# Kernel optimization log

Hardware: AMD Instinct MI355X
Metric: run time of the kernel (lower is better)

Reference implementation:

```python
import jax, jax.numpy as jnp
import numpy as np

B, T, F = 4, 8192, 1024
K = 4  # kernel_size

def setup_inputs() -> dict:
    key = jax.random.key(0)
    k1, k2 = jax.random.split(key)
    x = jax.random.normal(k1, (B, T, F), dtype=jnp.float32)
    # flax nnx.Conv depthwise kernel shape: (kernel_size, in_features//groups, out_features) = (K, 1, F)
    w = jax.random.normal(k2, (K, 1, F), dtype=jnp.float32) * (1.0 / np.sqrt(K))
    b = jnp.zeros((F,), dtype=jnp.float32)
    return {"x": x, "w": w, "b": b}

def reference(x, w, b):
    # Causal depthwise conv1d: pad left by K-1, groups=F.
    out = jax.lax.conv_general_dilated(
        x, w,
        window_strides=(1,),
        padding=[(K - 1, 0)],
        feature_group_count=F,
        dimension_numbers=("NWC", "WIO", "NWC"),
    )
    return out + b  # (B, T, F)
```

## Files before the change

### kernel.cpp

```cpp
#include <hip/hip_runtime.h>


constexpr int Bc = 4;
constexpr int Tc = 8192;
constexpr int Fc = 1024;
constexpr int Kc = 4;
constexpr int TCHUNK = 32;
constexpr int CHUNKS = Tc / TCHUNK;
constexpr int NBLK = Bc * CHUNKS;

__global__ __launch_bounds__(256) void causal_conv1d_kernel(
    const float* __restrict__ x,
    const float* __restrict__ w,
    const float* __restrict__ bias,
    float* __restrict__ out)
{
    const int f4  = threadIdx.x;
    const int f   = f4 * 4;
    const int bt  = blockIdx.x;
    const int b   = bt / CHUNKS;
    const int t0  = (bt % CHUNKS) * TCHUNK;

    const float4 w0 = *reinterpret_cast<const float4*>(w + 0 * Fc + f);
    const float4 w1 = *reinterpret_cast<const float4*>(w + 1 * Fc + f);
    const float4 w2 = *reinterpret_cast<const float4*>(w + 2 * Fc + f);
    const float4 w3 = *reinterpret_cast<const float4*>(w + 3 * Fc + f);
    const float4 bv = *reinterpret_cast<const float4*>(bias + f);

    const float* xp = x   + (size_t)b * Tc * Fc + f;
    float*       op = out + (size_t)b * Tc * Fc + f;

    float4 xm3, xm2, xm1;
    if (t0 >= 3) {
        xm3 = *reinterpret_cast<const float4*>(xp + (size_t)(t0 - 3) * Fc);
        xm2 = *reinterpret_cast<const float4*>(xp + (size_t)(t0 - 2) * Fc);
        xm1 = *reinterpret_cast<const float4*>(xp + (size_t)(t0 - 1) * Fc);
    } else {
        xm3 = make_float4(0.f, 0.f, 0.f, 0.f);
        xm2 = make_float4(0.f, 0.f, 0.f, 0.f);
        xm1 = make_float4(0.f, 0.f, 0.f, 0.f);
    }

#pragma unroll
    for (int i = 0; i < TCHUNK; ++i) {
        const int t = t0 + i;
        const float4 xc = *reinterpret_cast<const float4*>(xp + (size_t)t * Fc);

        float4 o;
        o.x = fmaf(w3.x, xc.x, fmaf(w2.x, xm1.x, fmaf(w1.x, xm2.x, fmaf(w0.x, xm3.x, bv.x))));
        o.y = fmaf(w3.y, xc.y, fmaf(w2.y, xm1.y, fmaf(w1.y, xm2.y, fmaf(w0.y, xm3.y, bv.y))));
        o.z = fmaf(w3.z, xc.z, fmaf(w2.z, xm1.z, fmaf(w1.z, xm2.z, fmaf(w0.z, xm3.z, bv.z))));
        o.w = fmaf(w3.w, xc.w, fmaf(w2.w, xm1.w, fmaf(w1.w, xm2.w, fmaf(w0.w, xm3.w, bv.w))));

        *reinterpret_cast<float4*>(op + (size_t)t * Fc) = o;

        xm3 = xm2;
        xm2 = xm1;
        xm1 = xc;
    }
}

extern "C" void kernel_launch(void* const* d_in, const int* in_sizes, int n_in,
                              void* d_out, int out_size, void* d_ws, size_t ws_size,
                              hipStream_t stream) {
    const float* x    = (const float*)d_in[0];
    const float* w    = (const float*)d_in[1];
    const float* bias = (const float*)d_in[2];
    float* out        = (float*)d_out;

    causal_conv1d_kernel<<<NBLK, 256, 0, stream>>>(x, w, bias, out);
}
```

Measured before the change: 239.3 us.

## Switch to grid-stride rows with per-row halo loads and XCD block swizzle

```diff
diff --git a/kernel.cpp b/kernel.cpp
--- a/kernel.cpp
+++ b/kernel.cpp
@@ -1,13 +1,13 @@
 #include <hip/hip_runtime.h>
 
 
-constexpr int Bc = 4;
-constexpr int Tc = 8192;
-constexpr int Fc = 1024;
-constexpr int Kc = 4;
-constexpr int TCHUNK = 32;
-constexpr int CHUNKS = Tc / TCHUNK;
-constexpr int NBLK = Bc * CHUNKS;
+constexpr int Tc   = 8192;
+constexpr int F4   = 256;
+constexpr int N4   = 4 * Tc * F4;
+constexpr int NBLK = 4096;
+constexpr int NTHR = 256;
+constexpr int ITERS = N4 / (NBLK * NTHR);
+constexpr int GSTRIDE = NBLK * NTHR;
 
 __global__ __launch_bounds__(256) void causal_conv1d_kernel(
     const float* __restrict__ x,
@@ -15,36 +15,39 @@
     const float* __restrict__ bias,
     float* __restrict__ out)
 {
-    const int f4  = threadIdx.x;
-    const int f   = f4 * 4;
-    const int bt  = blockIdx.x;
-    const int b   = bt / CHUNKS;
-    const int t0  = (bt % CHUNKS) * TCHUNK;
+    const int bid  = blockIdx.x;
+    const int wblk = (bid & 7) * (NBLK / 8) + (bid >> 3);
 
-    const float4 w0 = *reinterpret_cast<const float4*>(w + 0 * Fc + f);
-    const float4 w1 = *reinterpret_cast<const float4*>(w + 1 * Fc + f);
-    const float4 w2 = *reinterpret_cast<const float4*>(w + 2 * Fc + f);
-    const float4 w3 = *reinterpret_cast<const float4*>(w + 3 * Fc + f);
+    const int f  = threadIdx.x * 4;
+    const float4 w0 = *reinterpret_cast<const float4*>(w + 0 * 1024 + f);
+    const float4 w1 = *reinterpret_cast<const float4*>(w + 1 * 1024 + f);
+    const float4 w2 = *reinterpret_cast<const float4*>(w + 2 * 1024 + f);
+    const float4 w3 = *reinterpret_cast<const float4*>(w + 3 * 1024 + f);
     const float4 bv = *reinterpret_cast<const float4*>(bias + f);
 
-    const float* xp = x   + (size_t)b * Tc * Fc + f;
-    float*       op = out + (size_t)b * Tc * Fc + f;
+    const float4* __restrict__ x4 = reinterpret_cast<const float4*>(x);
+    float4* __restrict__ o4       = reinterpret_cast<float4*>(out);
 
-    float4 xm3, xm2, xm1;
-    if (t0 >= 3) {
-        xm3 = *reinterpret_cast<const float4*>(xp + (size_t)(t0 - 3) * Fc);
-        xm2 = *reinterpret_cast<const float4*>(xp + (size_t)(t0 - 2) * Fc);
-        xm1 = *reinterpret_cast<const float4*>(xp + (size_t)(t0 - 1) * Fc);
-    } else {
-        xm3 = make_float4(0.f, 0.f, 0.f, 0.f);
-        xm2 = make_float4(0.f, 0.f, 0.f, 0.f);
-        xm1 = make_float4(0.f, 0.f, 0.f, 0.f);
-    }
+    const int i0 = wblk * NTHR + threadIdx.x;
 
 #pragma unroll
-    for (int i = 0; i < TCHUNK; ++i) {
-        const int t = t0 + i;
-        const float4 xc = *reinterpret_cast<const float4*>(xp + (size_t)t * Fc);
+    for (int it = 0; it < ITERS; ++it) {
+        const int i = i0 + it * GSTRIDE;
+        const int t = (i >> 8) & (Tc - 1);
+
+        float4 xc, xm1, xm2, xm3;
+        if (t >= 3) {
+            xc  = x4[i];
+            xm1 = x4[i - 1 * F4];
+            xm2 = x4[i - 2 * F4];
+            xm3 = x4[i - 3 * F4];
+        } else {
+            const float4 z = make_float4(0.f, 0.f, 0.f, 0.f);
+            xc  = x4[i];
+            xm1 = (t >= 1) ? x4[i - 1 * F4] : z;
+            xm2 = (t >= 2) ? x4[i - 2 * F4] : z;
+            xm3 = z;
+        }
 
         float4 o;
         o.x = fmaf(w3.x, xc.x, fmaf(w2.x, xm1.x, fmaf(w1.x, xm2.x, fmaf(w0.x, xm3.x, bv.x))));
@@ -52,11 +55,7 @@
         o.z = fmaf(w3.z, xc.z, fmaf(w2.z, xm1.z, fmaf(w1.z, xm2.z, fmaf(w0.z, xm3.z, bv.z))));
         o.w = fmaf(w3.w, xc.w, fmaf(w2.w, xm1.w, fmaf(w1.w, xm2.w, fmaf(w0.w, xm3.w, bv.w))));
 
-        *reinterpret_cast<float4*>(op + (size_t)t * Fc) = o;
-
-        xm3 = xm2;
-        xm2 = xm1;
-        xm1 = xc;
+        o4[i] = o;
     }
 }
 
@@ -68,5 +67,5 @@
     const float* bias = (const float*)d_in[2];
     float* out        = (float*)d_out;
 
-    causal_conv1d_kernel<<<NBLK, 256, 0, stream>>>(x, w, bias, out);
+    causal_conv1d_kernel<<<NBLK, NTHR, 0, stream>>>(x, w, bias, out);
 }
```

Measured after the change: 244.7 us. 1.02x slower.
